# Performance work log

Measured on AMD Instinct MI355X. Metric: run time of the kernel, lower is better.

Reference implementation:

```python
import jax, jax.numpy as jnp
import numpy as np

N = 100000      # nodes
E = 1600000     # edges
NF, EF = 8, 4   # raw node/edge feature dims
HID = 64        # hidden_dim
HEADS = 4
C = HID // HEADS  # per-head channels = 16
L = 3           # num_layers
NEG_SLOPE = 0.2 # PyG GATConv leaky_relu slope
LN_EPS = 1e-5


def setup_inputs():
    key = jax.random.key(0)
    ks = jax.random.split(key, 16)
    s = 0.1
    return {
        "x": jax.random.normal(ks[0], (N, NF), dtype=jnp.float32),
        "edge_index": jax.random.randint(ks[1], (2, E), 0, N, dtype=jnp.int32),
        "edge_attr": jax.random.normal(ks[2], (E, EF), dtype=jnp.float32),
        "node_w": jax.random.normal(ks[3], (NF, HID), dtype=jnp.float32) * s,
        "node_b": jnp.zeros((HID,), jnp.float32),
        "edge_w": jax.random.normal(ks[4], (EF, HID), dtype=jnp.float32) * s,
        "edge_b": jnp.zeros((HID,), jnp.float32),
        "lin_w": jax.random.normal(ks[5], (L, HID, HEADS * C), dtype=jnp.float32) * s,
        "lin_edge_w": jax.random.normal(ks[6], (L, HID, HEADS * C), dtype=jnp.float32) * s,
        "att_src": jax.random.normal(ks[7], (L, HEADS, C), dtype=jnp.float32) * s,
        "att_dst": jax.random.normal(ks[8], (L, HEADS, C), dtype=jnp.float32) * s,
        "att_edge": jax.random.normal(ks[9], (L, HEADS, C), dtype=jnp.float32) * s,
        "gat_bias": jnp.zeros((L, HID), jnp.float32),
        "ln_gamma": jnp.ones((L, HID), jnp.float32),
        "ln_beta": jnp.zeros((L, HID), jnp.float32),
    }


def _layer_norm(x, g, b):
    mu = jnp.mean(x, axis=-1, keepdims=True)
    var = jnp.mean(jnp.square(x - mu), axis=-1, keepdims=True)
    return (x - mu) * jax.lax.rsqrt(var + LN_EPS) * g + b


def _gat_conv(x, src, dst, e_proj, lin_w, lin_edge_w, a_src_w, a_dst_w, a_edge_w, bias):
    """PyG GATConv (concat=True, edge_dim, self-loops with fill='mean').
    x: [N,HID]; src/dst: [E'] (already include self loops); e_proj: [E',HID]."""
    n = x.shape[0]
    xs = (x @ lin_w).reshape(n, HEADS, C)                    # [N,H,C]
    ea = (e_proj @ lin_edge_w).reshape(-1, HEADS, C)         # [E',H,C]
    a_src = jnp.einsum('nhc,hc->nh', xs, a_src_w)            # [N,H]
    a_dst = jnp.einsum('nhc,hc->nh', xs, a_dst_w)            # [N,H]
    a_edge = jnp.einsum('ehc,hc->eh', ea, a_edge_w)          # [E',H]
    alpha = a_src[src] + a_dst[dst] + a_edge                 # [E',H]
    alpha = jax.nn.leaky_relu(alpha, NEG_SLOPE)
    # segment softmax over edges sharing a destination node
    amax = jax.ops.segment_max(alpha, dst, num_segments=n)   # [N,H]
    ex = jnp.exp(alpha - amax[dst])
    denom = jax.ops.segment_sum(ex, dst, num_segments=n)     # [N,H]
    w = ex / (denom[dst] + 1e-16)                            # [E',H]
    msg = xs[src] * w[:, :, None]                            # [E',H,C]
    out = jax.ops.segment_sum(msg, dst, num_segments=n)      # [N,H,C]
    return out.reshape(n, HEADS * C) + bias


def reference(x, edge_index, edge_attr, node_w, node_b, edge_w, edge_b,
              lin_w, lin_edge_w, att_src, att_dst, att_edge, gat_bias,
              ln_gamma, ln_beta):
    h = x @ node_w + node_b                                  # [N,HID]
    e = edge_attr @ edge_w + edge_b                          # [E,HID]
    src, dst = edge_index[0], edge_index[1]
    # add self loops once (same for all layers); edge_attr fill = per-dst mean
    ones = jnp.ones((E,), h.dtype)
    deg = jax.ops.segment_sum(ones, dst, num_segments=N)     # [N]
    e_mean = jax.ops.segment_sum(e, dst, num_segments=N) / jnp.maximum(deg, 1.0)[:, None]
    loop = jnp.arange(N, dtype=src.dtype)
    src_f = jnp.concatenate([src, loop])
    dst_f = jnp.concatenate([dst, loop])
    e_f = jnp.concatenate([e, e_mean], axis=0)               # [E+N,HID]
    for i in range(L):
        residual = h
        h = _gat_conv(h, src_f, dst_f, e_f, lin_w[i], lin_edge_w[i],
                      att_src[i], att_dst[i], att_edge[i], gat_bias[i])
        h = _layer_norm(h + residual, ln_gamma[i], ln_beta[i])
        h = jax.nn.relu(h)
    return h
```

## Files before the change

### kernel.cpp

```cpp
#include <hip/hip_runtime.h>


#define LRELU_SLOPE 0.2f
#define LOG2E 1.4426950408889634f
#define P1B 512
#define NBKT_MAX 512

typedef float f32x2 __attribute__((ext_vector_type(2)));

#ifdef __has_builtin
#if __has_builtin(__builtin_amdgcn_fdot2_f32_bf16)
#define HAS_BF16DOT 1
#endif
#endif
#ifndef HAS_BF16DOT
#define HAS_BF16DOT 0
#endif

#if HAS_BF16DOT
typedef __bf16 bf16x2_t __attribute__((ext_vector_type(2)));
#endif

__device__ __forceinline__ f32x2 fp8lo(unsigned int v) {
    return __builtin_amdgcn_cvt_pk_f32_fp8((int)v, false);
}
__device__ __forceinline__ f32x2 fp8hi(unsigned int v) {
    return __builtin_amdgcn_cvt_pk_f32_fp8((int)v, true);
}
__device__ __forceinline__ ushort f2bf(float x) {
    unsigned int b = __float_as_uint(x);
    return (ushort)((b + 0x7fffu + ((b >> 16) & 1u)) >> 16);
}
__device__ __forceinline__ unsigned int pack2bf(float a, float b) {
    return (unsigned int)f2bf(a) | ((unsigned int)f2bf(b) << 16);
}
__device__ __forceinline__ float bf_lo(unsigned int v) { return __uint_as_float(v << 16); }
__device__ __forceinline__ float bf_hi(unsigned int v) { return __uint_as_float(v & 0xffff0000u); }

__device__ __forceinline__ float dot2bf(unsigned int a, unsigned int b, float c) {
#if HAS_BF16DOT
    return __builtin_amdgcn_fdot2_f32_bf16(__builtin_bit_cast(bf16x2_t, a),
                                           __builtin_bit_cast(bf16x2_t, b), c, false);
#else
    return fmaf(bf_lo(a), bf_lo(b), fmaf(bf_hi(a), bf_hi(b), c));
#endif
}

__global__ void k_prep0(const float* __restrict__ lin_edge_w,
                        const float* __restrict__ att_edge,
                        const float* __restrict__ edge_w,
                        const float* __restrict__ edge_b,
                        float* __restrict__ Mc,
                        const float* __restrict__ x, const float* __restrict__ nw,
                        const float* __restrict__ nb, ushort* __restrict__ hbf,
                        int n_nodes)
{
    __shared__ float we[3][64][4];
    int t = threadIdx.x;
    if (blockIdx.x == 0) {
        if (t < 192) {
            int l = t >> 6, k = t & 63;
            for (int h = 0; h < 4; ++h) {
                float acc = 0.f;
                #pragma unroll
                for (int c = 0; c < 16; ++c)
                    acc = fmaf(lin_edge_w[l*4096 + k*64 + h*16 + c],
                               att_edge[l*64 + h*16 + c], acc);
                we[l][k][h] = acc;
            }
        }
        __syncthreads();
        if (t < 48) {
            int l = t >> 4, k4 = (t >> 2) & 3, h = t & 3;
            float acc = 0.f;
            for (int k = 0; k < 64; ++k)
                acc = fmaf(edge_w[k4*64 + k], we[l][k][h], acc);
            Mc[l*16 + k4*4 + h] = acc * LOG2E;
        }
        if (t >= 64 && t < 76) {
            int u = t - 64, l = u >> 2, h = u & 3;
            float acc = 0.f;
            for (int k = 0; k < 64; ++k)
                acc = fmaf(edge_b[k], we[l][k][h], acc);
            Mc[48 + l*4 + h] = acc * LOG2E;
        }
        return;
    }
    int idx = (blockIdx.x - 1) * blockDim.x + t;
    int n = idx >> 6, j = idx & 63;
    if (n >= n_nodes) return;
    float acc = nb[j];
    #pragma unroll
    for (int k = 0; k < 8; ++k) acc = fmaf(x[n*8 + k], nw[k*64 + j], acc);
    hbf[(size_t)n*64 + j] = f2bf(acc);
}

__global__ __launch_bounds__(256) void k_hist1(const int* __restrict__ dst,
                                               int* __restrict__ C,
                                               int E, int chunk, int nbkt) {
    __shared__ int h[NBKT_MAX];
    int b = blockIdx.x, t = threadIdx.x;
    for (int i = t; i < nbkt; i += 256) h[i] = 0;
    __syncthreads();
    int e0 = b*chunk, e1 = min(e0 + chunk, E);
    for (int e = e0 + t; e < e1; e += 256)
        atomicAdd(&h[dst[e] >> 8], 1);
    __syncthreads();
    for (int i = t; i < nbkt; i += 256) C[i*P1B + b] = h[i];
}

__global__ void k_scanA(const int* __restrict__ in, int* __restrict__ out,
                        int* __restrict__ bsum, int n) {
    __shared__ int s[1024];
    int i = blockIdx.x*1024 + threadIdx.x;
    s[threadIdx.x] = (i < n) ? in[i] : 0;
    __syncthreads();
    for (int off = 1; off < 1024; off <<= 1) {
        int t = (threadIdx.x >= off) ? s[threadIdx.x - off] : 0;
        __syncthreads();
        s[threadIdx.x] += t;
        __syncthreads();
    }
    if (i < n) out[i] = s[threadIdx.x];
    if (threadIdx.x == 1023) bsum[blockIdx.x] = s[1023];
}

__global__ void k_scanB(int* bsum, int nb) {
    __shared__ int s[1024];
    int t = threadIdx.x;
    int own = (t < nb) ? bsum[t] : 0;
    s[t] = own;
    __syncthreads();
    for (int off = 1; off < 1024; off <<= 1) {
        int v = (t >= off) ? s[t - off] : 0;
        __syncthreads();
        s[t] += v;
        __syncthreads();
    }
    if (t < nb) bsum[t] = s[t] - own;
}

__device__ __forceinline__ int scanned(const int* S, const int* bsum, int idx) {
    return S[idx] + bsum[idx >> 10];
}

__global__ __launch_bounds__(256) void k_scat1(const int* __restrict__ dst,
        const int* __restrict__ srcv, const float4* __restrict__ ea,
        const int* __restrict__ S, const int* __restrict__ bsum,
        uint2* __restrict__ brec, int E, int chunk, int nbkt) {
    __shared__ int base[NBKT_MAX];
    __shared__ int cur[NBKT_MAX];
    int b = blockIdx.x, t = threadIdx.x;
    for (int i = t; i < nbkt; i += 256) {
        int flat = i*P1B + b;
        base[i] = flat ? scanned(S, bsum, flat - 1) : 0;
        cur[i] = 0;
    }
    __syncthreads();
    int e0 = b*chunk, e1 = min(e0 + chunk, E);
    for (int e = e0 + t; e < e1; e += 256) {
        int d = dst[e];
        int bin = d >> 8;
        int lr = atomicAdd(&cur[bin], 1);
        int slot = base[bin] + lr;
        float4 v = ea[e];
        unsigned int p = (unsigned int)__builtin_amdgcn_cvt_pk_fp8_f32(v.x, v.y, 0, false);
        p = (unsigned int)__builtin_amdgcn_cvt_pk_fp8_f32(v.z, v.w, (int)p, true);
        uint2 r;
        r.x = (unsigned int)srcv[e] | ((unsigned int)(d & 255) << 24);
        r.y = p;
        brec[slot] = r;
    }
}

__global__ __launch_bounds__(256) void k_csr(const uint2* __restrict__ brec,
        const int* __restrict__ S, const int* __restrict__ bsum,
        uint2* __restrict__ recs, int* __restrict__ rowptr, int* __restrict__ perm,
        int nbkt, int NN, int E) {
    int bkt = blockIdx.x, t = threadIdx.x;
    __shared__ int cnt[256], exc[256], cur[256], ssc[256];
    __shared__ int dh[64], dsc[64], dcu[64];
    int ib = bkt*P1B - 1, ie = (bkt + 1)*P1B - 1;
    int seg_b = bkt ? scanned(S, bsum, ib) : 0;
    int seg_e = scanned(S, bsum, ie);
    cnt[t] = 0; cur[t] = 0;
    if (t < 64) { dh[t] = 0; dcu[t] = 0; }
    __syncthreads();
    for (int i = seg_b + t; i < seg_e; i += 256)
        atomicAdd(&cnt[brec[i].x >> 24], 1);
    __syncthreads();
    ssc[t] = cnt[t];
    __syncthreads();
    for (int off = 1; off < 256; off <<= 1) {
        int v = (t >= off) ? ssc[t - off] : 0;
        __syncthreads();
        ssc[t] += v;
        __syncthreads();
    }
    exc[t] = ssc[t] - cnt[t];
    __syncthreads();
    int g = bkt*256 + t;
    bool valid = (g < NN);
    if (valid) rowptr[g] = seg_b + exc[t];
    if (bkt == nbkt - 1 && t == 0) rowptr[NN] = E;
    int dcl = valid ? min(cnt[t], 63) : 0;
    if (valid) atomicAdd(&dh[dcl], 1);
    __syncthreads();
    if (t < 64) dsc[t] = dh[t];
    __syncthreads();
    for (int off = 1; off < 64; off <<= 1) {
        int v = (t >= off && t < 64) ? dsc[t - off] : 0;
        __syncthreads();
        if (t < 64) dsc[t] += v;
        __syncthreads();
    }
    if (valid) {
        int slot = (dsc[dcl] - dh[dcl]) + atomicAdd(&dcu[dcl], 1);
        perm[bkt*256 + slot] = g;
    }
    for (int i = seg_b + t; i < seg_e; i += 256) {
        uint2 r = brec[i];
        int dl = (int)(r.x >> 24);
        int slot = seg_b + exc[dl] + atomicAdd(&cur[dl], 1);
        r.x &= 0x00FFFFFFu;
        recs[slot] = r;
    }
}

__global__ void k_eamean(const int* __restrict__ rowptr, const uint2* __restrict__ recs,
                         float4* __restrict__ ea_mean, int n) {
    int i = blockIdx.x*blockDim.x + threadIdx.x;
    if (i >= n) return;
    int b = rowptr[i], e = rowptr[i + 1];
    float sx = 0.f, sy = 0.f, sz = 0.f, sw = 0.f;
    for (int s = b; s < e; ++s) {
        unsigned int p = recs[s].y;
        f32x2 lo = fp8lo(p), hi = fp8hi(p);
        sx += lo.x; sy += lo.y; sz += hi.x; sw += hi.y;
    }
    float inv = (e > b) ? 1.f / (float)(e - b) : 0.f;
    ea_mean[i] = make_float4(sx*inv, sy*inv, sz*inv, sw*inv);
}

__global__ __launch_bounds__(256) void k_proj(const ushort* __restrict__ hbf,
        const float* __restrict__ lw,
        const float* __restrict__ asw,
        const float* __restrict__ adw,
        ushort* __restrict__ xs2, float* __restrict__ a_src4,
        float* __restrict__ a_dst4, int n_nodes)
{
    __shared__ unsigned int Wp[2048];
    for (int i = threadIdx.x; i < 2048; i += 256) {
        int k2 = i >> 6, c = i & 63;
        Wp[i] = pack2bf(lw[(k2*2)*64 + c], lw[(k2*2+1)*64 + c]);
    }
    __syncthreads();
    int lane = threadIdx.x & 63, wid = threadIdx.x >> 6;
    float as_w = asw[lane] * LOG2E, ad_w = adw[lane] * LOG2E;
    int nquads = (n_nodes + 3) >> 2;
    int nlast = n_nodes - 1;
    for (int q = blockIdx.x*4 + wid; q < nquads; q += gridDim.x*4) {
        int n0 = q << 2;
        int n1 = min(n0+1, nlast), n2 = min(n0+2, nlast), n3 = min(n0+3, nlast);
        const uint4* r0p = (const uint4*)(hbf + (size_t)n0*64);
        const uint4* r1p = (const uint4*)(hbf + (size_t)n1*64);
        const uint4* r2p = (const uint4*)(hbf + (size_t)n2*64);
        const uint4* r3p = (const uint4*)(hbf + (size_t)n3*64);
        float acc0 = 0.f, acc1 = 0.f, acc2 = 0.f, acc3 = 0.f;
        #pragma unroll
        for (int qq = 0; qq < 8; ++qq) {
            uint4 u0 = r0p[qq], u1 = r1p[qq], u2 = r2p[qq], u3 = r3p[qq];
            unsigned int w0 = Wp[(qq*4+0)*64 + lane];
            unsigned int w1 = Wp[(qq*4+1)*64 + lane];
            unsigned int w2 = Wp[(qq*4+2)*64 + lane];
            unsigned int w3 = Wp[(qq*4+3)*64 + lane];
            acc0 = dot2bf(u0.w, w3, dot2bf(u0.z, w2, dot2bf(u0.y, w1, dot2bf(u0.x, w0, acc0))));
            acc1 = dot2bf(u1.w, w3, dot2bf(u1.z, w2, dot2bf(u1.y, w1, dot2bf(u1.x, w0, acc1))));
            acc2 = dot2bf(u2.w, w3, dot2bf(u2.z, w2, dot2bf(u2.y, w1, dot2bf(u2.x, w0, acc2))));
            acc3 = dot2bf(u3.w, w3, dot2bf(u3.z, w2, dot2bf(u3.y, w1, dot2bf(u3.x, w0, acc3))));
        }
        xs2[(size_t)n0*64 + lane] = f2bf(acc0);
        xs2[(size_t)n1*64 + lane] = f2bf(acc1);
        xs2[(size_t)n2*64 + lane] = f2bf(acc2);
        xs2[(size_t)n3*64 + lane] = f2bf(acc3);
        #define ARED(ACC, NJ) { \
            float ps = (ACC)*as_w, pd = (ACC)*ad_w; \
            ps += __shfl_xor(ps,1,16); pd += __shfl_xor(pd,1,16); \
            ps += __shfl_xor(ps,2,16); pd += __shfl_xor(pd,2,16); \
            ps += __shfl_xor(ps,4,16); pd += __shfl_xor(pd,4,16); \
            ps += __shfl_xor(ps,8,16); pd += __shfl_xor(pd,8,16); \
            if ((lane & 15) == 0) { \
                a_src4[(NJ)*4 + (lane>>4)] = ps; \
                a_dst4[(NJ)*4 + (lane>>4)] = pd; \
            } }
        ARED(acc0, n0) ARED(acc1, n1) ARED(acc2, n2) ARED(acc3, n3)
        #undef ARED
    }
}

__global__ __launch_bounds__(256) void k_gat(const uint4* __restrict__ xs4,
        const float* __restrict__ a_src4, const float* __restrict__ a_dst4,
        const int* __restrict__ rowptr, const uint2* __restrict__ recs,
        const float4* __restrict__ ea_mean, const int* __restrict__ perm,
        const float* __restrict__ Mc,
        const float* __restrict__ c0,
        const float* __restrict__ bias, const float* __restrict__ lng,
        const float* __restrict__ lnb,
        const ushort* __restrict__ hbf_in, ushort* __restrict__ hbf_out,
        float* __restrict__ out_f32, int last, int n_nodes)
{
    int lane = threadIdx.x & 63;
    int g8 = lane >> 3;
    int gq = blockIdx.x*32 + (threadIdx.x >> 6)*8 + g8;
    bool active = (gq < n_nodes);
    int n = active ? perm[gq] : 0;
    int oct = lane & 7;
    int hB  = oct >> 1;
    int cb = oct * 8;
    uint4 rr = *(const uint4*)(hbf_in + (size_t)n*64 + cb);
    float4 eam = ea_mean[n];
    float m0 = Mc[hB], m1 = Mc[4+hB], m2 = Mc[8+hB], m3 = Mc[12+hB];
    float c0v = c0[hB];
    float adv = a_dst4[n*4 + hB];
    float cc = c0v + adv;
    int rb = rowptr[n], re = active ? rowptr[n + 1] : rb;

    float denL = 0.f;
    float a0=0.f,a1=0.f,a2=0.f,a3=0.f,a4=0.f,a5=0.f,a6=0.f,a7=0.f;

    if (rb < re) {
        int last_e = re - 1;
        uint2 rc = recs[rb];
        int i1 = min(rb + 1, last_e);
        uint2 rn = recs[i1];
        float asc = a_src4[(int)rc.x*4 + hB];
        uint4 xc = xs4[(unsigned)rc.x*8u + (unsigned)oct];
        #pragma unroll 2
        for (int b = rb; b < re; ++b) {
            int i2 = min(b + 2, last_e);
            uint2 r2 = recs[i2];
            float asn = a_src4[(int)rn.x*4 + hB];
            uint4 xn = xs4[(unsigned)rn.x*8u + (unsigned)oct];
            f32x2 e01 = fp8lo(rc.y), e23 = fp8hi(rc.y);
            float al = fmaf(e01.x, m0, fmaf(e01.y, m1,
                       fmaf(e23.x, m2, fmaf(e23.y, m3, cc)))) + asc;
            al = fmaxf(al, LRELU_SLOPE * al);
            float ev = exp2f(al);
            denL += ev;
            a0 = fmaf(bf_lo(xc.x), ev, a0); a1 = fmaf(bf_hi(xc.x), ev, a1);
            a2 = fmaf(bf_lo(xc.y), ev, a2); a3 = fmaf(bf_hi(xc.y), ev, a3);
            a4 = fmaf(bf_lo(xc.z), ev, a4); a5 = fmaf(bf_hi(xc.z), ev, a5);
            a6 = fmaf(bf_lo(xc.w), ev, a6); a7 = fmaf(bf_hi(xc.w), ev, a7);
            rc = rn; rn = r2; asc = asn; xc = xn;
        }
    }
    float ael = (re > rb)
        ? fmaf(eam.x, m0, fmaf(eam.y, m1, fmaf(eam.z, m2, fmaf(eam.w, m3, c0v))))
        : 0.f;
    float alS = a_src4[n*4 + hB] + adv + ael;
    alS = fmaxf(alS, LRELU_SLOPE * alS);
    float evS = exp2f(alS);
    float denF = denL + evS;
    uint4 vs = xs4[(unsigned)n*8u + (unsigned)oct];
    a0 = fmaf(bf_lo(vs.x), evS, a0); a1 = fmaf(bf_hi(vs.x), evS, a1);
    a2 = fmaf(bf_lo(vs.y), evS, a2); a3 = fmaf(bf_hi(vs.y), evS, a3);
    a4 = fmaf(bf_lo(vs.z), evS, a4); a5 = fmaf(bf_hi(vs.z), evS, a5);
    a6 = fmaf(bf_lo(vs.w), evS, a6); a7 = fmaf(bf_hi(vs.w), evS, a7);
    float inv = 1.f / (denF + 1e-16f);
    const float4* bp = (const float4*)(bias + cb);
    float4 b0 = bp[0], b1 = bp[1];
    float o0 = a0*inv + b0.x + bf_lo(rr.x), o1 = a1*inv + b0.y + bf_hi(rr.x);
    float o2 = a2*inv + b0.z + bf_lo(rr.y), o3 = a3*inv + b0.w + bf_hi(rr.y);
    float o4 = a4*inv + b1.x + bf_lo(rr.z), o5 = a5*inv + b1.y + bf_hi(rr.z);
    float o6 = a6*inv + b1.z + bf_lo(rr.w), o7 = a7*inv + b1.w + bf_hi(rr.w);
    float s1 = o0+o1+o2+o3+o4+o5+o6+o7;
    s1 += __shfl_xor(s1, 1); s1 += __shfl_xor(s1, 2); s1 += __shfl_xor(s1, 4);
    float mu = s1 * 0.015625f;
    float d0=o0-mu,d1=o1-mu,d2=o2-mu,d3=o3-mu,d4=o4-mu,d5=o5-mu,d6=o6-mu,d7=o7-mu;
    float s2 = d0*d0+d1*d1+d2*d2+d3*d3+d4*d4+d5*d5+d6*d6+d7*d7;
    s2 += __shfl_xor(s2, 1); s2 += __shfl_xor(s2, 2); s2 += __shfl_xor(s2, 4);
    float rs = rsqrtf(s2 * 0.015625f + 1e-5f);
    const float4* gp = (const float4*)(lng + cb);
    const float4* zp = (const float4*)(lnb + cb);
    float4 g0 = gp[0], g1 = gp[1], z0 = zp[0], z1 = zp[1];
    float y0 = fmaxf(d0*rs*g0.x + z0.x, 0.f), y1 = fmaxf(d1*rs*g0.y + z0.y, 0.f);
    float y2 = fmaxf(d2*rs*g0.z + z0.z, 0.f), y3 = fmaxf(d3*rs*g0.w + z0.w, 0.f);
    float y4 = fmaxf(d4*rs*g1.x + z1.x, 0.f), y5 = fmaxf(d5*rs*g1.y + z1.y, 0.f);
    float y6 = fmaxf(d6*rs*g1.z + z1.z, 0.f), y7 = fmaxf(d7*rs*g1.w + z1.w, 0.f);
    if (active) {
        if (last) {
            float4* outp = (float4*)(out_f32 + (size_t)n*64 + cb);
            outp[0] = make_float4(y0, y1, y2, y3);
            outp[1] = make_float4(y4, y5, y6, y7);
        } else {
            uint4 pk;
            pk.x = pack2bf(y0, y1); pk.y = pack2bf(y2, y3);
            pk.z = pack2bf(y4, y5); pk.w = pack2bf(y6, y7);
            *(uint4*)(hbf_out + (size_t)n*64 + cb) = pk;
        }
    }
}

extern "C" void kernel_launch(void* const* d_in, const int* in_sizes, int n_in,
                              void* d_out, int out_size, void* d_ws, size_t ws_size,
                              hipStream_t stream) {
    const float* x          = (const float*)d_in[0];
    const int*   ei         = (const int*)d_in[1];
    const float* edge_attr  = (const float*)d_in[2];
    const float* node_w     = (const float*)d_in[3];
    const float* node_b     = (const float*)d_in[4];
    const float* edge_w     = (const float*)d_in[5];
    const float* edge_b     = (const float*)d_in[6];
    const float* lin_w      = (const float*)d_in[7];
    const float* lin_edge_w = (const float*)d_in[8];
    const float* att_src    = (const float*)d_in[9];
    const float* att_dst    = (const float*)d_in[10];
    const float* att_edge   = (const float*)d_in[11];
    const float* gat_bias   = (const float*)d_in[12];
    const float* ln_g       = (const float*)d_in[13];
    const float* ln_b       = (const float*)d_in[14];

    int NN = in_sizes[0] / 8;
    int E  = in_sizes[1] / 2;
    const int* src = ei;
    const int* dst = ei + E;

    int nbkt = (NN + 255) >> 8;
    int ntot = nbkt * P1B;
    int chunk = (E + P1B - 1) / P1B;

    char* wsp = (char*)d_ws;
    size_t off = 0;
    auto alloc = [&](size_t bytes) -> void* {
        off = (off + 255) & ~(size_t)255;
        void* p = wsp + off;
        off += bytes;
        return p;
    };
    ushort* h_bf    = (ushort*)alloc((size_t)NN * 64 * 2);
    ushort* xs2     = (ushort*)alloc((size_t)NN * 64 * 2);
    float*  a_src4  = (float*)alloc((size_t)NN * 4 * 4);
    float*  a_dst4  = (float*)alloc((size_t)NN * 4 * 4);
    uint2*  recs    = (uint2*)alloc((size_t)E * 8);
    uint2*  brec    = (uint2*)alloc((size_t)E * 8);
    float4* ea_mean = (float4*)alloc((size_t)NN * 16);
    int*    rowptr  = (int*)alloc((size_t)(NN + 1) * 4);
    int*    perm    = (int*)alloc((size_t)NN * 4);
    int*    S       = (int*)alloc((size_t)ntot * 4);
    int*    bsum    = (int*)alloc(4096);
    float*  Mc      = (float*)alloc(256);

    k_prep0<<<1 + (NN*64 + 255) / 256, 256, 0, stream>>>(
        lin_edge_w, att_edge, edge_w, edge_b, Mc, x, node_w, node_b, h_bf, NN);
    k_hist1<<<P1B, 256, 0, stream>>>(dst, S, E, chunk, nbkt);
    int nsb = (ntot + 1023) / 1024;
    k_scanA<<<nsb, 1024, 0, stream>>>(S, S, bsum, ntot);
    k_scanB<<<1, 1024, 0, stream>>>(bsum, nsb);
    k_scat1<<<P1B, 256, 0, stream>>>(dst, src, (const float4*)edge_attr,
                                     S, bsum, brec, E, chunk, nbkt);
    k_csr<<<nbkt, 256, 0, stream>>>(brec, S, bsum, recs, rowptr, perm, nbkt, NN, E);
    k_eamean<<<(NN + 255) / 256, 256, 0, stream>>>(rowptr, recs, ea_mean, NN);

    for (int l = 0; l < 3; ++l) {
        k_proj<<<2048, 256, 0, stream>>>(h_bf, lin_w + l*4096, att_src + l*64,
                                         att_dst + l*64, xs2, a_src4, a_dst4, NN);
        k_gat<<<(NN + 31) / 32, 256, 0, stream>>>((const uint4*)xs2, a_src4, a_dst4,
                                                  rowptr, recs, ea_mean, perm,
                                                  Mc + l*16, Mc + 48 + l*4,
                                                  gat_bias + l*64, ln_g + l*64, ln_b + l*64,
                                                  h_bf, h_bf, (float*)d_out,
                                                  (l == 2) ? 1 : 0, NN);
    }
}
```

Before: 375.8 us.

## Split each node's edge loop across two 8-lane groups in GAT aggregation

The GAT aggregation kernel now assigns 16 lanes per destination node instead of 8. The two 8-lane halves process alternate edges and combine their partial softmax numerators and denominators with cross-lane shuffles. This shortens the serial per-node gather chain and raises memory-level parallelism on the random row gathers. In exchange it doubles the launched thread count, adds shuffle reductions, and idles half the lanes during the LayerNorm epilogue.

```diff
diff --git a/kernel.cpp b/kernel.cpp
--- a/kernel.cpp
+++ b/kernel.cpp
@@ -310,13 +310,15 @@
         float* __restrict__ out_f32, int last, int n_nodes)
 {
     int lane = threadIdx.x & 63;
-    int g8 = lane >> 3;
-    int gq = blockIdx.x*32 + (threadIdx.x >> 6)*8 + g8;
+    int q4 = lane >> 4;
+    int gq = blockIdx.x*16 + (threadIdx.x >> 6)*4 + q4;
     bool active = (gq < n_nodes);
     int n = active ? perm[gq] : 0;
-    int oct = lane & 7;
-    int hB  = oct >> 1;
-    int cb = oct * 8;
+    int l4  = lane & 15;
+    int k8  = l4 & 7;
+    int hB  = k8 >> 1;
+    int grp = l4 >> 3;
+    int cb = k8 * 8;
     uint4 rr = *(const uint4*)(hbf_in + (size_t)n*64 + cb);
     float4 eam = ea_mean[n];
     float m0 = Mc[hB], m1 = Mc[4+hB], m2 = Mc[8+hB], m3 = Mc[12+hB];
@@ -330,22 +332,23 @@
 
     if (rb < re) {
         int last_e = re - 1;
-        uint2 rc = recs[rb];
-        int i1 = min(rb + 1, last_e);
+        int i0 = rb + grp;     i0 = (i0 > last_e) ? last_e : i0;
+        uint2 rc = recs[i0];
+        int i1 = rb + 2 + grp; i1 = (i1 > last_e) ? last_e : i1;
         uint2 rn = recs[i1];
         float asc = a_src4[(int)rc.x*4 + hB];
-        uint4 xc = xs4[(unsigned)rc.x*8u + (unsigned)oct];
+        uint4 xc = xs4[(unsigned)rc.x*8u + (unsigned)k8];
         #pragma unroll 2
-        for (int b = rb; b < re; ++b) {
-            int i2 = min(b + 2, last_e);
+        for (int b = rb; b < re; b += 2) {
+            int i2 = b + 4 + grp; i2 = (i2 > last_e) ? last_e : i2;
             uint2 r2 = recs[i2];
             float asn = a_src4[(int)rn.x*4 + hB];
-            uint4 xn = xs4[(unsigned)rn.x*8u + (unsigned)oct];
+            uint4 xn = xs4[(unsigned)rn.x*8u + (unsigned)k8];
             f32x2 e01 = fp8lo(rc.y), e23 = fp8hi(rc.y);
             float al = fmaf(e01.x, m0, fmaf(e01.y, m1,
                        fmaf(e23.x, m2, fmaf(e23.y, m3, cc)))) + asc;
             al = fmaxf(al, LRELU_SLOPE * al);
-            float ev = exp2f(al);
+            float ev = (b + grp < re) ? exp2f(al) : 0.f;
             denL += ev;
             a0 = fmaf(bf_lo(xc.x), ev, a0); a1 = fmaf(bf_hi(xc.x), ev, a1);
             a2 = fmaf(bf_lo(xc.y), ev, a2); a3 = fmaf(bf_hi(xc.y), ev, a3);
@@ -354,6 +357,11 @@
             rc = rn; rn = r2; asc = asn; xc = xn;
         }
     }
+    denL += __shfl_xor(denL, 8);
+    a0 += __shfl_xor(a0, 8); a1 += __shfl_xor(a1, 8);
+    a2 += __shfl_xor(a2, 8); a3 += __shfl_xor(a3, 8);
+    a4 += __shfl_xor(a4, 8); a5 += __shfl_xor(a5, 8);
+    a6 += __shfl_xor(a6, 8); a7 += __shfl_xor(a7, 8);
     float ael = (re > rb)
         ? fmaf(eam.x, m0, fmaf(eam.y, m1, fmaf(eam.z, m2, fmaf(eam.w, m3, c0v))))
         : 0.f;
@@ -361,7 +369,7 @@
     alS = fmaxf(alS, LRELU_SLOPE * alS);
     float evS = exp2f(alS);
     float denF = denL + evS;
-    uint4 vs = xs4[(unsigned)n*8u + (unsigned)oct];
+    uint4 vs = xs4[(unsigned)n*8u + (unsigned)k8];
     a0 = fmaf(bf_lo(vs.x), evS, a0); a1 = fmaf(bf_hi(vs.x), evS, a1);
     a2 = fmaf(bf_lo(vs.y), evS, a2); a3 = fmaf(bf_hi(vs.y), evS, a3);
     a4 = fmaf(bf_lo(vs.z), evS, a4); a5 = fmaf(bf_hi(vs.z), evS, a5);
@@ -387,7 +395,7 @@
     float y2 = fmaxf(d2*rs*g0.z + z0.z, 0.f), y3 = fmaxf(d3*rs*g0.w + z0.w, 0.f);
     float y4 = fmaxf(d4*rs*g1.x + z1.x, 0.f), y5 = fmaxf(d5*rs*g1.y + z1.y, 0.f);
     float y6 = fmaxf(d6*rs*g1.z + z1.z, 0.f), y7 = fmaxf(d7*rs*g1.w + z1.w, 0.f);
-    if (active) {
+    if (grp == 0 && active) {
         if (last) {
             float4* outp = (float4*)(out_f32 + (size_t)n*64 + cb);
             outp[0] = make_float4(y0, y1, y2, y3);
@@ -464,7 +472,7 @@
     for (int l = 0; l < 3; ++l) {
         k_proj<<<2048, 256, 0, stream>>>(h_bf, lin_w + l*4096, att_src + l*64,
                                          att_dst + l*64, xs2, a_src4, a_dst4, NN);
-        k_gat<<<(NN + 31) / 32, 256, 0, stream>>>((const uint4*)xs2, a_src4, a_dst4,
+        k_gat<<<(NN + 15) / 16, 256, 0, stream>>>((const uint4*)xs2, a_src4, a_dst4,
                                                   rowptr, recs, ea_mean, perm,
                                                   Mc + l*16, Mc + 48 + l*4,
                                                   gat_bias + l*64, ln_g + l*64, ln_b + l*64,
```

Result: faster. 352.8 us (-6.1%).
